# Optimization experiments

Measured on AMD Instinct MI355X. Metric: run time of the kernel, lower is better.

The kernel has to match this reference:

```python
import jax, jax.numpy as jnp
import numpy as np

EPS_GN = 1e-8
EPS_ATTN = 1e-8


def setup_inputs() -> dict:
    key = jax.random.key(0)
    ks = jax.random.split(key, 13)
    B, C, N = 4, 512, 2048
    s = 0.02
    return {
        "x": jax.random.normal(ks[0], (B, C, N), jnp.float32),
        "dw_w": jax.random.normal(ks[1], (C, 3), jnp.float32) * s,
        "pw_w": jax.random.normal(ks[2], (C, C), jnp.float32) * s,
        "u_w": jax.random.normal(ks[3], (2 * C, C), jnp.float32) * s,
        "u_b": jax.random.normal(ks[4], (2 * C,), jnp.float32) * s,
        "v_w": jax.random.normal(ks[5], (2 * C, C), jnp.float32) * s,
        "v_b": jax.random.normal(ks[6], (2 * C,), jnp.float32) * s,
        "h_w": jax.random.normal(ks[7], (C, C), jnp.float32) * s,
        "h_b": jax.random.normal(ks[8], (C,), jnp.float32) * s,
        "q_w": jax.random.normal(ks[9], (C, C), jnp.float32) * s,
        "k_w": jax.random.normal(ks[10], (C, C), jnp.float32) * s,
        "o_w": jax.random.normal(ks[11], (C, 2 * C), jnp.float32) * s,
        "o_b": jax.random.normal(ks[12], (C,), jnp.float32) * s,
    }


def reference(x, dw_w, pw_w, u_w, u_b, v_w, v_b, h_w, h_b, q_w, k_w, o_w, o_b):
    # x: [B, C, N]
    C = x.shape[1]
    # GroupNorm(1, C): normalize over (C, N) per sample; affine is identity-init
    # in torch but we follow the module math with default weight=1, bias=0
    mean = jnp.mean(x, axis=(1, 2), keepdims=True)
    var = jnp.var(x, axis=(1, 2), keepdims=True)
    z = (x - mean) * jax.lax.rsqrt(var + EPS_GN)

    # local depthwise conv k=3, pad=1 (cross-correlation), no bias
    zp = jnp.pad(z, ((0, 0), (0, 0), (1, 1)))
    dw = (dw_w[:, 0, None] * zp[:, :, :-2]
          + dw_w[:, 1, None] * zp[:, :, 1:-1]
          + dw_w[:, 2, None] * zp[:, :, 2:])
    # pointwise conv (no bias)
    z = z + jnp.einsum('oc,bcn->bon', pw_w, dw)

    u = jax.nn.sigmoid(jnp.einsum('oc,bcn->bon', u_w, z) + u_b[:, None])  # [B,2C,N]
    v = jnp.einsum('oc,bcn->bon', v_w, z) + v_b[:, None]                  # [B,2C,N]
    h = jnp.einsum('oc,bcn->bno', h_w, z) + h_b                           # [B,N,C]

    q = h @ q_w.T  # [B,N,C]
    k = h @ k_w.T  # [B,N,C]
    scale = 1.0 / jnp.sqrt(jnp.float32(C))

    logits = jnp.einsum('bnc,bmc->bnm', q, k) * scale
    a = jax.nn.relu(logits)
    a = a * a
    a = a / (jnp.sum(a, axis=-1, keepdims=True) + EPS_ATTN)

    av = jnp.einsum('bnm,bom->bon', a, v)  # [B,2C,N]
    y = jnp.einsum('oc,bcn->bon', o_w, u * av) + o_b[:, None]
    return x + y
```

## Files before the change

kernel.cpp:

```cpp
#include <hip/hip_runtime.h>
#include <hip/hip_bf16.h>
#include <cstdint>

typedef __bf16 bhalf;
typedef __bf16 bhalf8 __attribute__((ext_vector_type(8)));
typedef float f32x4 __attribute__((ext_vector_type(4)));

enum { EPI_Z2=0, EPI_UV=1, EPI_BIAS=2, EPI_QK=3, EPI_ATTN=4, EPI_PV=5, EPI_Y=6 };

__device__ __forceinline__ void gl_lds16(const bhalf* g, bhalf* l) {
  __builtin_amdgcn_global_load_lds(
      (const __attribute__((address_space(1))) unsigned int*)g,
      (__attribute__((address_space(3))) unsigned int*)l,
      16, 0, 0);
}
__device__ __forceinline__ void barrier_raw() { asm volatile("s_barrier" ::: "memory"); }
#define VMW(n)  asm volatile("s_waitcnt vmcnt(" #n ")" ::: "memory")
#define LGKM0() asm volatile("s_waitcnt lgkmcnt(0)" ::: "memory")


template<int EPI>
__global__ void __launch_bounds__(512, 4)
gemm256(const bhalf* __restrict__ A, const bhalf* __restrict__ Bw,
        void* __restrict__ Out, void* __restrict__ Out2,
        const float* __restrict__ bias, const float* __restrict__ bias2,
        const bhalf* __restrict__ auxb, const float* __restrict__ auxf,
        int N, int K, long sA, long sB, long sO, long sAuxf,
        float scale, int rowshift)
{
  constexpr int ABUF = 256*64;
  constexpr int BBUF = 128*64;
  constexpr int STRIDE = ABUF + BBUF;
  __shared__ __align__(16) char lds[3*STRIDE];

  const int gx = gridDim.x, gy = gridDim.y;
  const int nwg = gx*gy;
  const int flat = blockIdx.y*gx + blockIdx.x;
  const int q8 = nwg>>3, r8 = nwg&7, xcd = flat&7, o8 = flat>>3;
  const int wsw = (xcd<r8 ? xcd*(q8+1) : r8*(q8+1)+(xcd-r8)*q8) + o8;
  const int bx = wsw % gx, by = wsw / gx;
  const int m0 = by*256, n0 = bx*128;
  const int bz = blockIdx.z;

  const bhalf* Ab = A + (long)bz*sA;
  const bhalf* Bb = Bw + (rowshift ? (long)(m0>>rowshift)*sB : (long)bz*sB);

  const int tid = threadIdx.x, wid = tid>>6, lane = tid&63;
  const int lm = lane&15, kq = lane>>4;
  const int wm = wid>>2, wn = wid&3;
  const int srow = lane>>2;
  const int csw = ((lane&3) ^ ((lane>>3)&3)) * 8;
  const int kqs = kq ^ ((lm>>1)&3);

  f32x4 acc[8][2];
  #pragma unroll
  for (int i=0;i<8;i++)
    #pragma unroll
    for (int j=0;j<2;j++) acc[i][j] = f32x4{0.f,0.f,0.f,0.f};

  auto stage = [&](int buf, int t){
    char* base = lds + buf*STRIDE;
    const int k0 = t*32;
    #pragma unroll
    for (int c=0;c<2;c++){
      bhalf* d = (bhalf*)(base + (wid*32 + c*16)*64);
      gl_lds16(Ab + (long)(m0 + wid*32 + c*16 + srow)*K + k0 + csw, d);
    }
    bhalf* d = (bhalf*)(base + ABUF + (wid*16)*64);
    gl_lds16(Bb + (long)(n0 + wid*16 + srow)*K + k0 + csw, d);
  };

  auto compute = [&](int buf){
    char* base = lds + buf*STRIDE;
    bhalf8 af[8], bf[2];
    #pragma unroll
    for (int i=0;i<8;i++)
      af[i] = *(const bhalf8*)(base + (wm*128 + i*16 + lm)*64 + kqs*16);
    #pragma unroll
    for (int j=0;j<2;j++)
      bf[j] = *(const bhalf8*)(base + ABUF + (wn*32 + j*16 + lm)*64 + kqs*16);
    __builtin_amdgcn_s_setprio(1);
    #pragma unroll
    for (int i=0;i<8;i++)
      #pragma unroll
      for (int j=0;j<2;j++)
        acc[i][j] = __builtin_amdgcn_mfma_f32_16x16x32_bf16(af[i], bf[j], acc[i][j], 0,0,0);
    __builtin_amdgcn_s_setprio(0);
  };

  const int NT = K>>5;
  stage(0,0); stage(1,1);
  int b0 = 0;
  for (int t=0; t<NT; ++t){
    if (t+2<NT){
      int b2 = b0+2; if (b2>=3) b2-=3;
      stage(b2, t+2);
      VMW(6);
    } else if (t+1<NT) { VMW(3); }
    else               { VMW(0); }
    barrier_raw();
    compute(b0);
    barrier_raw();
    if (++b0==3) b0=0;
  }

  char* obase; int ldb;
  const float* bv = nullptr; int bc0 = 0; bool sig = false;
  if constexpr (EPI==EPI_ATTN){
    obase = (char*)Out + 2*((long)bz*sO + (long)m0*N + n0); ldb = N*2;
  }
  if constexpr (EPI==EPI_PV){
    obase = (char*)Out + 2*((long)m0*1024 + n0); ldb = 2048;
  }
  if constexpr (EPI==EPI_UV){
    bool uh = n0 < 1024; sig = uh;
    obase = (char*)(uh?Out:Out2) + 2*((long)m0*1024 + (n0 - (uh?0:1024)));
    ldb = 2048; bv = uh ? bias : bias2; bc0 = uh ? n0 : n0-1024;
  }
  if constexpr (EPI==EPI_QK){
    bool qh = n0 < 512;
    obase = (char*)(qh?Out:Out2) + 2*((long)m0*512 + (n0 - (qh?0:512)));
    ldb = 1024;
  }

  float rs[8][4];
  if constexpr (EPI==EPI_ATTN){
    #pragma unroll
    for (int i=0;i<8;i++)
      #pragma unroll
      for (int r=0;r<4;r++) rs[i][r]=0.f;
  }
  #pragma unroll
  for (int i=0;i<8;i++){
    #pragma unroll
    for (int j=0;j<2;j++){
      const int lcol = wn*32 + j*16 + lm;
      #pragma unroll
      for (int r=0;r<4;r++){
        const int lrow = wm*128 + i*16 + kq*4 + r;
        float v = acc[i][j][r];
        if constexpr (EPI==EPI_ATTN){
          v *= scale; v = fmaxf(v,0.f); v = v*v;
          rs[i][r] += v;
        }
        if constexpr (EPI==EPI_PV){
          const int rowg = m0 + lrow;
          float den = auxf[rowg];
          v *= __builtin_amdgcn_rcpf(den + 1e-8f);
          v *= (float)auxb[(long)rowg*1024 + n0 + lcol];
        }
        if constexpr (EPI==EPI_UV){
          v += bv[bc0 + lcol];
          if (sig) v = 1.f/(1.f + __expf(-v));
        }
        const int cb = lcol*2;
        const int lb = lrow*256 + (((cb>>5) ^ ((lrow>>2)&3))<<5) + (cb&31);
        *(bhalf*)(lds + lb) = (bhalf)v;
      }
    }
  }
  if constexpr (EPI==EPI_ATTN){
    float* rd = (float*)Out2;
    #pragma unroll
    for (int i=0;i<8;i++){
      const int rbase = m0 + wm*128 + i*16 + kq*4;
      #pragma unroll
      for (int r=0;r<4;r++){
        float s = rs[i][r];
        s += __shfl_xor(s,1); s += __shfl_xor(s,2);
        s += __shfl_xor(s,4); s += __shfl_xor(s,8);
        if (lm==0) atomicAdd(rd + (long)bz*sAuxf + rbase + r, s);
      }
    }
  }
  LGKM0();
  barrier_raw();
  #pragma unroll
  for (int it=0; it<8; ++it){
    const int g = (it*512 + tid)*16;
    const int row = g >> 8, off = g & 255;
    const int lb = row*256 + (((off>>5) ^ ((row>>2)&3))<<5) + (off&31);
    uint4 val = *(const uint4*)(lds + lb);
    *(uint4*)(obase + (long)row*ldb + off) = val;
  }
  (void)scale; (void)bias; (void)bias2; (void)auxb; (void)auxf; (void)N;
}

template<int EPI>
__global__ void __launch_bounds__(256, 2)
gemm_bt(const bhalf* __restrict__ A, const bhalf* __restrict__ Bw,
        void* __restrict__ Out,
        const float* __restrict__ bias,
        const bhalf* __restrict__ auxb,
        int M, int N, int K, long sA, long sB)
{
  constexpr int ABUF = 128*64;
  constexpr int STRIDE = 2*ABUF;
  __shared__ __align__(16) char lds[4*STRIDE];

  const int bz = blockIdx.z;
  const int gx = gridDim.x, gy = gridDim.y;
  const int nwg = gx*gy;
  const int flat = blockIdx.y*gx + blockIdx.x;
  const int q8 = nwg>>3, r8 = nwg&7, xcd = flat&7, o8 = flat>>3;
  const int w = (xcd<r8 ? xcd*(q8+1) : r8*(q8+1)+(xcd-r8)*q8) + o8;
  const int bx = w % gx, by = w / gx;

  const bhalf* Ab = A + (long)bz*sA;
  const bhalf* Bb = Bw + (long)bz*sB;
  const int tid = threadIdx.x;
  const int wid = tid>>6, lane = tid&63;
  const int lm = lane&15, kq = lane>>4;
  const int wr = (wid>>1)*64, wc = (wid&1)*64;
  const int m0 = by*128, n0 = bx*128;
  const int srow = lane>>2;
  const int csw = ((lane&3) ^ ((lane>>3)&3))*8;
  const int kqs = kq ^ ((lm>>1)&3);

  f32x4 acc[4][4];
  #pragma unroll
  for (int i=0;i<4;i++)
    #pragma unroll
    for (int j=0;j<4;j++) acc[i][j] = f32x4{0.f,0.f,0.f,0.f};

  auto stage = [&](int t){
    char* base = lds + (t&3)*STRIDE;
    const int k0 = t*32;
    #pragma unroll
    for (int c=0;c<2;c++){
      bhalf* dA = (bhalf*)(base + (wid*32 + c*16)*64);
      gl_lds16(Ab + (long)(m0 + wid*32 + c*16 + srow)*K + k0 + csw, dA);
      bhalf* dB = (bhalf*)(base + ABUF + (wid*32 + c*16)*64);
      gl_lds16(Bb + (long)(n0 + wid*32 + c*16 + srow)*K + k0 + csw, dB);
    }
  };

  auto compute = [&](int t){
    char* base = lds + (t&3)*STRIDE;
    bhalf8 af[4], bf[4];
    #pragma unroll
    for (int i=0;i<4;i++)
      af[i] = *(const bhalf8*)(base + (wr + i*16 + lm)*64 + kqs*16);
    #pragma unroll
    for (int j=0;j<4;j++)
      bf[j] = *(const bhalf8*)(base + ABUF + (wc + j*16 + lm)*64 + kqs*16);
    __builtin_amdgcn_s_setprio(1);
    #pragma unroll
    for (int i=0;i<4;i++)
      #pragma unroll
      for (int j=0;j<4;j++)
        acc[i][j] = __builtin_amdgcn_mfma_f32_16x16x32_bf16(af[i], bf[j], acc[i][j], 0,0,0);
    __builtin_amdgcn_s_setprio(0);
  };

  const int NT = K>>5;
  stage(0); stage(1); stage(2);
  for (int t=0; t<NT; ++t){
    if (t+3<NT){ stage(t+3); VMW(12); }
    else if (t+2<NT) { VMW(8); }
    else if (t+1<NT) { VMW(4); }
    else             { VMW(0); }
    barrier_raw();
    compute(t);
    barrier_raw();
  }

  char* obase = (char*)Out + 2*((long)m0*N + n0);
  const int ldb = N*2;
  #pragma unroll
  for (int i=0;i<4;i++){
    #pragma unroll
    for (int j=0;j<4;j++){
      const int lcol = wc + j*16 + lm;
      #pragma unroll
      for (int r=0;r<4;r++){
        const int lrow = wr + i*16 + kq*4 + r;
        float v = acc[i][j][r];
        if constexpr (EPI==EPI_Z2)
          v += (float)auxb[(long)(m0+lrow)*N + n0 + lcol];
        if constexpr (EPI==EPI_BIAS || EPI==EPI_Y)
          v += bias[n0 + lcol];
        const int cb = lcol*2;
        const int lb = lrow*256 + (((cb>>5) ^ ((lrow>>2)&3))<<5) + (cb&31);
        *(bhalf*)(lds + lb) = (bhalf)v;
      }
    }
  }
  LGKM0();
  barrier_raw();
  #pragma unroll
  for (int it=0; it<8; ++it){
    const int g = (it*256 + tid)*16;
    const int row = g >> 8, off = g & 255;
    const int lb = row*256 + (((off>>5) ^ ((row>>2)&3))<<5) + (off&31);
    uint4 val = *(const uint4*)(lds + lb);
    *(uint4*)(obase + (long)row*ldb + off) = val;
  }
  (void)M;
}

struct CvtArgs { const float* src[7]; bhalf* dst[7]; int n[7]; };
__global__ void cvt_multi(CvtArgs a) {
  int seg = blockIdx.y;
  int i = (blockIdx.x*256 + threadIdx.x)*4;
  if (i >= a.n[seg]) return;
  float4 f = *(const float4*)(a.src[seg] + i);
  bhalf* d = a.dst[seg] + i;
  d[0]=(bhalf)f.x; d[1]=(bhalf)f.y; d[2]=(bhalf)f.z; d[3]=(bhalf)f.w;
}

__global__ void gn_part(const float* __restrict__ x, float* __restrict__ ps, float* __restrict__ pss) {
  int b = blockIdx.y;
  const float* xb = x + (long)b*(512*2048);
  float s=0.f, ss=0.f;
  #pragma unroll
  for (int it=0; it<8; it++){
    int idx = ((it*128 + blockIdx.x)*256 + threadIdx.x)*4;
    float4 f = *(const float4*)(xb + idx);
    s  += f.x+f.y+f.z+f.w;
    ss += f.x*f.x+f.y*f.y+f.z*f.z+f.w*f.w;
  }
  for (int off=32; off; off>>=1){ s += __shfl_xor(s,off); ss += __shfl_xor(ss,off); }
  __shared__ float ls[4], lss[4];
  int wid = threadIdx.x>>6, lane = threadIdx.x&63;
  if (lane==0){ ls[wid]=s; lss[wid]=ss; }
  __syncthreads();
  if (threadIdx.x==0){
    s = ls[0]+ls[1]+ls[2]+ls[3]; ss = lss[0]+lss[1]+lss[2]+lss[3];
    ps[b*128 + blockIdx.x] = s; pss[b*128 + blockIdx.x] = ss;
  }
}

__global__ void gn_final(const float* __restrict__ ps, const float* __restrict__ pss,
                         float* __restrict__ stats) {
  int b = blockIdx.x;
  float s = ps[b*128 + threadIdx.x], ss = pss[b*128 + threadIdx.x];
  for (int off=32; off; off>>=1){ s += __shfl_xor(s,off); ss += __shfl_xor(ss,off); }
  __shared__ float l0[2], l1[2];
  int wid = threadIdx.x>>6, lane = threadIdx.x&63;
  if (lane==0){ l0[wid]=s; l1[wid]=ss; }
  __syncthreads();
  if (threadIdx.x==0){
    s = l0[0]+l0[1]; ss = l1[0]+l1[1];
    float mean = s*(1.f/1048576.f);
    float var  = ss*(1.f/1048576.f) - mean*mean;
    stats[b*2] = mean; stats[b*2+1] = rsqrtf(var + 1e-8f);
  }
}

__global__ void norm_dw_T(const float* __restrict__ x, const float* __restrict__ stats,
                          const float* __restrict__ dw_w,
                          bhalf* __restrict__ zT, bhalf* __restrict__ dwT) {
  int b = blockIdx.z, n0 = blockIdx.x*32, c0 = blockIdx.y*32;
  float mean = stats[b*2], rstd = stats[b*2+1];
  __shared__ float zs[32][35];
  int tx = threadIdx.x, ty = threadIdx.y;
  #pragma unroll
  for (int r=0;r<4;r++){
    int c = c0 + ty + r*8;
    for (int cc=tx; cc<34; cc+=32){
      int n = n0 - 1 + cc;
      float v = 0.f;
      if (n>=0 && n<2048) v = (x[((long)b*512 + c)*2048 + n] - mean)*rstd;
      zs[ty + r*8][cc] = v;
    }
  }
  __syncthreads();
  float w0 = dw_w[(c0+tx)*3+0], w1 = dw_w[(c0+tx)*3+1], w2 = dw_w[(c0+tx)*3+2];
  #pragma unroll
  for (int r=0;r<4;r++){
    int ln = ty + r*8;
    float z = zs[tx][ln+1];
    float d = w0*zs[tx][ln] + w1*zs[tx][ln+1] + w2*zs[tx][ln+2];
    long o = ((long)b*2048 + n0 + ln)*512 + c0 + tx;
    zT[o] = (bhalf)z; dwT[o] = (bhalf)d;
  }
}

__global__ void transpose_bf16(const bhalf* __restrict__ in, bhalf* __restrict__ out,
                               int R, int C) {
  __shared__ bhalf t[32][33];
  int r0 = blockIdx.x*32, c0 = blockIdx.y*32;
  long ib = (long)blockIdx.z*R*C;
  int tx = threadIdx.x, ty = threadIdx.y;
  #pragma unroll
  for (int r=0;r<4;r++)
    t[ty + r*8][tx] = in[ib + (long)(r0 + ty + r*8)*C + c0 + tx];
  __syncthreads();
  #pragma unroll
  for (int r=0;r<4;r++)
    out[ib + (long)(c0 + ty + r*8)*R + r0 + tx] = t[tx][ty + r*8];
}

__global__ void final_add(const float* __restrict__ x, const bhalf* __restrict__ yT,
                          float* __restrict__ out) {
  __shared__ float t[32][33];
  int n0 = blockIdx.x*32, c0 = blockIdx.y*32, b = blockIdx.z;
  int tx = threadIdx.x, ty = threadIdx.y;
  #pragma unroll
  for (int r=0;r<4;r++)
    t[ty + r*8][tx] = (float)yT[((long)b*2048 + n0 + ty + r*8)*512 + c0 + tx];
  __syncthreads();
  #pragma unroll
  for (int r=0;r<4;r++){
    long idx = ((long)b*512 + c0 + ty + r*8)*2048 + n0 + tx;
    out[idx] = x[idx] + t[tx][ty + r*8];
  }
}

extern "C" void kernel_launch(void* const* d_in, const int* in_sizes, int n_in,
                              void* d_out, int out_size, void* d_ws, size_t ws_size,
                              hipStream_t stream) {
  (void)in_sizes; (void)n_in; (void)out_size; (void)ws_size;
  const float* x    = (const float*)d_in[0];
  const float* dw_w = (const float*)d_in[1];
  const float* pw_w = (const float*)d_in[2];
  const float* u_w  = (const float*)d_in[3];
  const float* u_b  = (const float*)d_in[4];
  const float* v_w  = (const float*)d_in[5];
  const float* v_b  = (const float*)d_in[6];
  const float* h_w  = (const float*)d_in[7];
  const float* h_b  = (const float*)d_in[8];
  const float* q_w  = (const float*)d_in[9];
  const float* k_w  = (const float*)d_in[10];
  const float* o_w  = (const float*)d_in[11];
  const float* o_b  = (const float*)d_in[12];
  float* out = (float*)d_out;

  char* ws = (char*)d_ws;
  size_t off = 0;
  auto alloc = [&](size_t bytes) -> void* {
    void* p = ws + off; off = (off + bytes + 255) & ~(size_t)255; return p;
  };

  float* ps    = (float*)alloc(4*128*4);
  float* pss   = (float*)alloc(4*128*4);
  float* stats = (float*)alloc(4*2*4);
  float* rden  = (float*)alloc(4*2048*4);
  bhalf* wb_pw = (bhalf*)alloc(512*512*2);
  bhalf* wb_uv = (bhalf*)alloc((size_t)2048*512*2);
  bhalf* wb_h  = (bhalf*)alloc(512*512*2);
  bhalf* wb_qk = (bhalf*)alloc((size_t)1024*512*2);
  bhalf* wb_o  = (bhalf*)alloc((size_t)512*1024*2);
  const size_t ACT = (size_t)4*2048*512;
  bhalf* zT   = (bhalf*)alloc(ACT*2);
  bhalf* dwT  = (bhalf*)alloc(ACT*2);
  bhalf* z2T  = (bhalf*)alloc(ACT*2);
  bhalf* ub   = (bhalf*)alloc(ACT*2*2);
  bhalf* vT   = (bhalf*)alloc(ACT*2*2);
  bhalf* v_fm = (bhalf*)alloc(ACT*2*2);
  bhalf* hb   = (bhalf*)alloc(ACT*2);
  bhalf* wsc  = (bhalf*)alloc((size_t)4*2048*2048*2);
  bhalf* uav  = (bhalf*)alloc(ACT*2*2);
  bhalf* qb = zT;  bhalf* kb = dwT;  bhalf* yT = vT;

  hipMemsetAsync(rden, 0, 4*2048*4, stream);

  CvtArgs ca;
  ca.src[0]=pw_w; ca.dst[0]=wb_pw;           ca.n[0]=512*512;
  ca.src[1]=u_w;  ca.dst[1]=wb_uv;           ca.n[1]=1024*512;
  ca.src[2]=v_w;  ca.dst[2]=wb_uv+1024*512;  ca.n[2]=1024*512;
  ca.src[3]=h_w;  ca.dst[3]=wb_h;            ca.n[3]=512*512;
  ca.src[4]=q_w;  ca.dst[4]=wb_qk;           ca.n[4]=512*512;
  ca.src[5]=k_w;  ca.dst[5]=wb_qk+512*512;   ca.n[5]=512*512;
  ca.src[6]=o_w;  ca.dst[6]=wb_o;            ca.n[6]=512*1024;
  cvt_multi<<<dim3(512,7), 256, 0, stream>>>(ca);

  gn_part<<<dim3(128,4), 256, 0, stream>>>(x, ps, pss);
  gn_final<<<dim3(4), 128, 0, stream>>>(ps, pss, stats);

  norm_dw_T<<<dim3(64,16,4), dim3(32,8), 0, stream>>>(x, stats, dw_w, zT, dwT);

  const float iscl = 0.044194173824159216f;
  gemm_bt<EPI_Z2><<<dim3(4,64,1), 256, 0, stream>>>(dwT, wb_pw, z2T,
      nullptr, zT, 8192, 512, 512, 0, 0);
  gemm256<EPI_UV><<<dim3(16,32,1), 512, 0, stream>>>(z2T, wb_uv, ub, vT,
      u_b, v_b, nullptr, nullptr, 2048, 512, 0,0,0,0, 0.f, 0);
  gemm_bt<EPI_BIAS><<<dim3(4,64,1), 256, 0, stream>>>(z2T, wb_h, hb,
      h_b, nullptr, 8192, 512, 512, 0, 0);
  gemm256<EPI_QK><<<dim3(8,32,1), 512, 0, stream>>>(hb, wb_qk, qb, kb,
      nullptr, nullptr, nullptr, nullptr, 1024, 512, 0,0,0,0, 0.f, 0);
  transpose_bf16<<<dim3(64,32,4), dim3(32,8), 0, stream>>>(vT, v_fm, 2048, 1024);
  gemm256<EPI_ATTN><<<dim3(16,8,4), 512, 0, stream>>>(qb, kb, wsc, rden,
      nullptr, nullptr, nullptr, nullptr, 2048, 512,
      (long)2048*512, (long)2048*512, (long)2048*2048, 2048, iscl, 0);
  gemm256<EPI_PV><<<dim3(8,32,1), 512, 0, stream>>>(wsc, v_fm, uav, nullptr,
      nullptr, nullptr, ub, rden, 1024, 2048,
      0, (long)1024*2048, 0, 0, 0.f, 11);
  gemm_bt<EPI_Y><<<dim3(4,64,1), 256, 0, stream>>>(uav, wb_o, yT,
      o_b, nullptr, 8192, 512, 1024, 0, 0);
  final_add<<<dim3(64,16,4), dim3(32,8), 0, stream>>>(x, yT, out);
}
```

Before: 208.3 us.

## Split GEMM into 256x256 and 4-wave 256x128 variants with larger per-wave tiles

Replaces the single 256x128 GEMM kernel with two variants. g8 uses 256x256 output tiles, 512 threads, a BK=64 double buffer, and 8x4 MFMA tiles per wave, and serves the UV projection and attention-score GEMMs. g4 keeps 256x128 tiles but runs them with 4 waves, each holding a 128x64 accumulator, and serves the QK and PV GEMMs. Both raise the MFMA work done per LDS fragment load and halve the grid for the large GEMMs. The cost is roughly twice the accumulator registers per wave, which lowers occupancy (launch bounds drop to 2), plus more LDS per block and fewer blocks to spread across CUs.

```diff
diff --git a/kernel.cpp b/kernel.cpp
--- a/kernel.cpp
+++ b/kernel.cpp
@@ -20,13 +20,162 @@
 
 
 template<int EPI>
-__global__ void __launch_bounds__(512, 4)
-gemm256(const bhalf* __restrict__ A, const bhalf* __restrict__ Bw,
-        void* __restrict__ Out, void* __restrict__ Out2,
-        const float* __restrict__ bias, const float* __restrict__ bias2,
-        const bhalf* __restrict__ auxb, const float* __restrict__ auxf,
-        int N, int K, long sA, long sB, long sO, long sAuxf,
-        float scale, int rowshift)
+__global__ void __launch_bounds__(512, 2)
+g8(const bhalf* __restrict__ A, const bhalf* __restrict__ Bw,
+   void* __restrict__ Out, void* __restrict__ Out2,
+   const float* __restrict__ bias, const float* __restrict__ bias2,
+   int N, int K, long sA, long sB, long sO, long sAuxf, float scale)
+{
+  constexpr int ASL = 256*64;
+  constexpr int ABUF = 2*ASL;
+  constexpr int STRIDE = 2*ABUF;
+  __shared__ __align__(16) char lds[2*STRIDE];
+
+  const int gx = gridDim.x, gy = gridDim.y;
+  const int nwg = gx*gy;
+  const int flat = blockIdx.y*gx + blockIdx.x;
+  const int q8 = nwg>>3, r8 = nwg&7, xcd = flat&7, o8 = flat>>3;
+  const int wsw = (xcd<r8 ? xcd*(q8+1) : r8*(q8+1)+(xcd-r8)*q8) + o8;
+  const int bx = wsw % gx, by = wsw / gx;
+  const int m0 = by*256, n0 = bx*256;
+  const int bz = blockIdx.z;
+
+  const bhalf* Ab = A + (long)bz*sA;
+  const bhalf* Bb = Bw + (long)bz*sB;
+
+  const int tid = threadIdx.x, wid = tid>>6, lane = tid&63;
+  const int lm = lane&15, kq = lane>>4;
+  const int wm = wid>>2, wn = wid&3;
+  const int srow = lane>>2;
+  const int csw = ((lane&3) ^ ((lane>>3)&3)) * 8;
+  const int kqs = kq ^ ((lm>>1)&3);
+
+  f32x4 acc[8][4];
+  #pragma unroll
+  for (int i=0;i<8;i++)
+    #pragma unroll
+    for (int j=0;j<4;j++) acc[i][j] = f32x4{0.f,0.f,0.f,0.f};
+
+  auto stage = [&](int buf, int t){
+    char* base = lds + buf*STRIDE;
+    const int k0 = t*64;
+    #pragma unroll
+    for (int ksl=0; ksl<2; ksl++){
+      #pragma unroll
+      for (int c=0;c<2;c++){
+        bhalf* dA = (bhalf*)(base + ksl*ASL + (wid*32 + c*16)*64);
+        gl_lds16(Ab + (long)(m0 + wid*32 + c*16 + srow)*K + k0 + ksl*32 + csw, dA);
+        bhalf* dB = (bhalf*)(base + ABUF + ksl*ASL + (wid*32 + c*16)*64);
+        gl_lds16(Bb + (long)(n0 + wid*32 + c*16 + srow)*K + k0 + ksl*32 + csw, dB);
+      }
+    }
+  };
+
+  auto compute = [&](int buf){
+    char* base = lds + buf*STRIDE;
+    #pragma unroll
+    for (int ks=0; ks<2; ks++){
+      bhalf8 af[8], bf[4];
+      #pragma unroll
+      for (int i=0;i<8;i++)
+        af[i] = *(const bhalf8*)(base + ks*ASL + (wm*128 + i*16 + lm)*64 + kqs*16);
+      #pragma unroll
+      for (int j=0;j<4;j++)
+        bf[j] = *(const bhalf8*)(base + ABUF + ks*ASL + (wn*64 + j*16 + lm)*64 + kqs*16);
+      __builtin_amdgcn_s_setprio(1);
+      #pragma unroll
+      for (int i=0;i<8;i++)
+        #pragma unroll
+        for (int j=0;j<4;j++)
+          acc[i][j] = __builtin_amdgcn_mfma_f32_16x16x32_bf16(af[i], bf[j], acc[i][j], 0,0,0);
+      __builtin_amdgcn_s_setprio(0);
+    }
+  };
+
+  const int NT = K>>6;
+  stage(0,0);
+  for (int t=0; t<NT; ++t){
+    if (t+1<NT){ stage((t+1)&1, t+1); VMW(8); }
+    else       { VMW(0); }
+    barrier_raw();
+    compute(t&1);
+    barrier_raw();
+  }
+
+  char* obase; int ldb;
+  const float* bv = nullptr; int bc0 = 0; bool sig = false;
+  if constexpr (EPI==EPI_ATTN){
+    obase = (char*)Out + 2*((long)bz*sO + (long)m0*N + n0); ldb = N*2;
+  }
+  if constexpr (EPI==EPI_UV){
+    bool uh = n0 < 1024; sig = uh;
+    obase = (char*)(uh?Out:Out2) + 2*((long)m0*1024 + (n0 - (uh?0:1024)));
+    ldb = 2048; bv = uh ? bias : bias2; bc0 = uh ? n0 : n0-1024;
+  }
+
+  float rs[8][4];
+  if constexpr (EPI==EPI_ATTN){
+    #pragma unroll
+    for (int i=0;i<8;i++)
+      #pragma unroll
+      for (int r=0;r<4;r++) rs[i][r]=0.f;
+  }
+  #pragma unroll
+  for (int i=0;i<8;i++){
+    #pragma unroll
+    for (int j=0;j<4;j++){
+      const int lcol = wn*64 + j*16 + lm;
+      #pragma unroll
+      for (int r=0;r<4;r++){
+        const int lrow = wm*128 + i*16 + kq*4 + r;
+        float v = acc[i][j][r];
+        if constexpr (EPI==EPI_ATTN){
+          v *= scale; v = fmaxf(v,0.f); v = v*v;
+          rs[i][r] += v;
+        }
+        if constexpr (EPI==EPI_UV){
+          v += bv[bc0 + lcol];
+          if (sig) v = 1.f/(1.f + __expf(-v));
+        }
+        const int cb = lcol*2;
+        const int lb = lrow*512 + (((cb>>5) ^ ((lrow>>2)&3))<<5) + (cb&31);
+        *(bhalf*)(lds + lb) = (bhalf)v;
+      }
+    }
+  }
+  if constexpr (EPI==EPI_ATTN){
+    float* rd = (float*)Out2;
+    #pragma unroll
+    for (int i=0;i<8;i++){
+      const int rbase = m0 + wm*128 + i*16 + kq*4;
+      #pragma unroll
+      for (int r=0;r<4;r++){
+        float s = rs[i][r];
+        s += __shfl_xor(s,1); s += __shfl_xor(s,2);
+        s += __shfl_xor(s,4); s += __shfl_xor(s,8);
+        if (lm==0) atomicAdd(rd + (long)bz*sAuxf + rbase + r, s);
+      }
+    }
+  }
+  LGKM0();
+  barrier_raw();
+  #pragma unroll
+  for (int it=0; it<16; ++it){
+    const int g = (it*512 + tid)*16;
+    const int row = g >> 9, off = g & 511;
+    const int lb = row*512 + (((off>>5) ^ ((row>>2)&3))<<5) + (off&31);
+    uint4 val = *(const uint4*)(lds + lb);
+    *(uint4*)(obase + (long)row*ldb + off) = val;
+  }
+  (void)scale; (void)bias; (void)bias2; (void)N;
+}
+
+template<int EPI>
+__global__ void __launch_bounds__(256, 2)
+g4(const bhalf* __restrict__ A, const bhalf* __restrict__ Bw,
+   void* __restrict__ Out, void* __restrict__ Out2,
+   const bhalf* __restrict__ auxb, const float* __restrict__ auxf,
+   int N, int K, long sA, long sB, long sO, float scale, int rowshift)
 {
   constexpr int ABUF = 256*64;
   constexpr int BBUF = 128*64;
@@ -47,43 +196,46 @@
 
   const int tid = threadIdx.x, wid = tid>>6, lane = tid&63;
   const int lm = lane&15, kq = lane>>4;
-  const int wm = wid>>2, wn = wid&3;
+  const int wm = wid>>1, wn = wid&1;
   const int srow = lane>>2;
   const int csw = ((lane&3) ^ ((lane>>3)&3)) * 8;
   const int kqs = kq ^ ((lm>>1)&3);
 
-  f32x4 acc[8][2];
+  f32x4 acc[8][4];
   #pragma unroll
   for (int i=0;i<8;i++)
     #pragma unroll
-    for (int j=0;j<2;j++) acc[i][j] = f32x4{0.f,0.f,0.f,0.f};
+    for (int j=0;j<4;j++) acc[i][j] = f32x4{0.f,0.f,0.f,0.f};
 
   auto stage = [&](int buf, int t){
     char* base = lds + buf*STRIDE;
     const int k0 = t*32;
     #pragma unroll
+    for (int c=0;c<4;c++){
+      bhalf* dA = (bhalf*)(base + (wid*64 + c*16)*64);
+      gl_lds16(Ab + (long)(m0 + wid*64 + c*16 + srow)*K + k0 + csw, dA);
+    }
+    #pragma unroll
     for (int c=0;c<2;c++){
-      bhalf* d = (bhalf*)(base + (wid*32 + c*16)*64);
-      gl_lds16(Ab + (long)(m0 + wid*32 + c*16 + srow)*K + k0 + csw, d);
-    }
-    bhalf* d = (bhalf*)(base + ABUF + (wid*16)*64);
-    gl_lds16(Bb + (long)(n0 + wid*16 + srow)*K + k0 + csw, d);
+      bhalf* dB = (bhalf*)(base + ABUF + (wid*32 + c*16)*64);
+      gl_lds16(Bb + (long)(n0 + wid*32 + c*16 + srow)*K + k0 + csw, dB);
+    }
   };
 
   auto compute = [&](int buf){
     char* base = lds + buf*STRIDE;
-    bhalf8 af[8], bf[2];
+    bhalf8 af[8], bf[4];
     #pragma unroll
     for (int i=0;i<8;i++)
       af[i] = *(const bhalf8*)(base + (wm*128 + i*16 + lm)*64 + kqs*16);
     #pragma unroll
-    for (int j=0;j<2;j++)
-      bf[j] = *(const bhalf8*)(base + ABUF + (wn*32 + j*16 + lm)*64 + kqs*16);
+    for (int j=0;j<4;j++)
+      bf[j] = *(const bhalf8*)(base + ABUF + (wn*64 + j*16 + lm)*64 + kqs*16);
     __builtin_amdgcn_s_setprio(1);
     #pragma unroll
     for (int i=0;i<8;i++)
       #pragma unroll
-      for (int j=0;j<2;j++)
+      for (int j=0;j<4;j++)
         acc[i][j] = __builtin_amdgcn_mfma_f32_16x16x32_bf16(af[i], bf[j], acc[i][j], 0,0,0);
     __builtin_amdgcn_s_setprio(0);
   };
@@ -95,8 +247,8 @@
     if (t+2<NT){
       int b2 = b0+2; if (b2>=3) b2-=3;
       stage(b2, t+2);
-      VMW(6);
-    } else if (t+1<NT) { VMW(3); }
+      VMW(12);
+    } else if (t+1<NT) { VMW(6); }
     else               { VMW(0); }
     barrier_raw();
     compute(b0);
@@ -105,85 +257,46 @@
   }
 
   char* obase; int ldb;
-  const float* bv = nullptr; int bc0 = 0; bool sig = false;
-  if constexpr (EPI==EPI_ATTN){
-    obase = (char*)Out + 2*((long)bz*sO + (long)m0*N + n0); ldb = N*2;
-  }
   if constexpr (EPI==EPI_PV){
     obase = (char*)Out + 2*((long)m0*1024 + n0); ldb = 2048;
-  }
-  if constexpr (EPI==EPI_UV){
-    bool uh = n0 < 1024; sig = uh;
-    obase = (char*)(uh?Out:Out2) + 2*((long)m0*1024 + (n0 - (uh?0:1024)));
-    ldb = 2048; bv = uh ? bias : bias2; bc0 = uh ? n0 : n0-1024;
   }
   if constexpr (EPI==EPI_QK){
     bool qh = n0 < 512;
     obase = (char*)(qh?Out:Out2) + 2*((long)m0*512 + (n0 - (qh?0:512)));
     ldb = 1024;
   }
-
-  float rs[8][4];
-  if constexpr (EPI==EPI_ATTN){
-    #pragma unroll
-    for (int i=0;i<8;i++)
-      #pragma unroll
-      for (int r=0;r<4;r++) rs[i][r]=0.f;
-  }
   #pragma unroll
   for (int i=0;i<8;i++){
     #pragma unroll
-    for (int j=0;j<2;j++){
-      const int lcol = wn*32 + j*16 + lm;
+    for (int j=0;j<4;j++){
+      const int lcol = wn*64 + j*16 + lm;
       #pragma unroll
       for (int r=0;r<4;r++){
         const int lrow = wm*128 + i*16 + kq*4 + r;
         float v = acc[i][j][r];
-        if constexpr (EPI==EPI_ATTN){
-          v *= scale; v = fmaxf(v,0.f); v = v*v;
-          rs[i][r] += v;
-        }
         if constexpr (EPI==EPI_PV){
           const int rowg = m0 + lrow;
           float den = auxf[rowg];
           v *= __builtin_amdgcn_rcpf(den + 1e-8f);
           v *= (float)auxb[(long)rowg*1024 + n0 + lcol];
         }
-        if constexpr (EPI==EPI_UV){
-          v += bv[bc0 + lcol];
-          if (sig) v = 1.f/(1.f + __expf(-v));
-        }
         const int cb = lcol*2;
         const int lb = lrow*256 + (((cb>>5) ^ ((lrow>>2)&3))<<5) + (cb&31);
         *(bhalf*)(lds + lb) = (bhalf)v;
       }
     }
   }
-  if constexpr (EPI==EPI_ATTN){
-    float* rd = (float*)Out2;
-    #pragma unroll
-    for (int i=0;i<8;i++){
-      const int rbase = m0 + wm*128 + i*16 + kq*4;
-      #pragma unroll
-      for (int r=0;r<4;r++){
-        float s = rs[i][r];
-        s += __shfl_xor(s,1); s += __shfl_xor(s,2);
-        s += __shfl_xor(s,4); s += __shfl_xor(s,8);
-        if (lm==0) atomicAdd(rd + (long)bz*sAuxf + rbase + r, s);
-      }
-    }
-  }
   LGKM0();
   barrier_raw();
   #pragma unroll
-  for (int it=0; it<8; ++it){
-    const int g = (it*512 + tid)*16;
+  for (int it=0; it<16; ++it){
+    const int g = (it*256 + tid)*16;
     const int row = g >> 8, off = g & 255;
     const int lb = row*256 + (((off>>5) ^ ((row>>2)&3))<<5) + (off&31);
     uint4 val = *(const uint4*)(lds + lb);
     *(uint4*)(obase + (long)row*ldb + off) = val;
   }
-  (void)scale; (void)bias; (void)bias2; (void)auxb; (void)auxf; (void)N;
+  (void)scale; (void)auxb; (void)auxf; (void)N; (void)sO;
 }
 
 template<int EPI>
@@ -474,19 +587,18 @@
   const float iscl = 0.044194173824159216f;
   gemm_bt<EPI_Z2><<<dim3(4,64,1), 256, 0, stream>>>(dwT, wb_pw, z2T,
       nullptr, zT, 8192, 512, 512, 0, 0);
-  gemm256<EPI_UV><<<dim3(16,32,1), 512, 0, stream>>>(z2T, wb_uv, ub, vT,
-      u_b, v_b, nullptr, nullptr, 2048, 512, 0,0,0,0, 0.f, 0);
+  g8<EPI_UV><<<dim3(8,32,1), 512, 0, stream>>>(z2T, wb_uv, ub, vT,
+      u_b, v_b, 2048, 512, 0, 0, 0, 0, 0.f);
   gemm_bt<EPI_BIAS><<<dim3(4,64,1), 256, 0, stream>>>(z2T, wb_h, hb,
       h_b, nullptr, 8192, 512, 512, 0, 0);
-  gemm256<EPI_QK><<<dim3(8,32,1), 512, 0, stream>>>(hb, wb_qk, qb, kb,
-      nullptr, nullptr, nullptr, nullptr, 1024, 512, 0,0,0,0, 0.f, 0);
+  g4<EPI_QK><<<dim3(8,32,1), 256, 0, stream>>>(hb, wb_qk, qb, kb,
+      nullptr, nullptr, 1024, 512, 0, 0, 0, 0.f, 0);
   transpose_bf16<<<dim3(64,32,4), dim3(32,8), 0, stream>>>(vT, v_fm, 2048, 1024);
-  gemm256<EPI_ATTN><<<dim3(16,8,4), 512, 0, stream>>>(qb, kb, wsc, rden,
-      nullptr, nullptr, nullptr, nullptr, 2048, 512,
-      (long)2048*512, (long)2048*512, (long)2048*2048, 2048, iscl, 0);
-  gemm256<EPI_PV><<<dim3(8,32,1), 512, 0, stream>>>(wsc, v_fm, uav, nullptr,
-      nullptr, nullptr, ub, rden, 1024, 2048,
-      0, (long)1024*2048, 0, 0, 0.f, 11);
+  g8<EPI_ATTN><<<dim3(8,8,4), 512, 0, stream>>>(qb, kb, wsc, rden,
+      nullptr, nullptr, 2048, 512,
+      (long)2048*512, (long)2048*512, (long)2048*2048, 2048, iscl);
+  g4<EPI_PV><<<dim3(8,32,1), 256, 0, stream>>>(wsc, v_fm, uav, nullptr,
+      ub, rden, 1024, 2048, 0, (long)1024*2048, 0, 0.f, 11);
   gemm_bt<EPI_Y><<<dim3(4,64,1), 256, 0, stream>>>(uav, wb_o, yT,
       o_b, nullptr, 8192, 512, 1024, 0, 0);
   final_add<<<dim3(64,16,4), dim3(32,8), 0, stream>>>(x, yT, out);
```

Result: no change. 210.2 us (+0.9%).
